# Optimization experiments

Hardware: AMD Instinct MI355X
Metric: run time of the kernel (lower is better)

## Reference

```python
import jax, jax.numpy as jnp
import numpy as np

ALPHA = 0.2  # LeakyReLU negative slope
NEG = -9e15


def _gat_heads(x, adj_mask, W, a):
    # x: (B,N,F); W: (H,F,O); a: (H,2O); adj_mask: (B,N,N) bool
    O = W.shape[-1]
    Wh = jnp.einsum('bnf,hfo->bhno', x, W)            # (B,H,N,O)
    e1 = jnp.einsum('bhno,ho->bhn', Wh, a[:, :O])     # Wh @ a[:O]
    e2 = jnp.einsum('bhno,ho->bhn', Wh, a[:, O:])     # Wh @ a[O:]
    e = jax.nn.leaky_relu(e1[:, :, :, None] + e2[:, :, None, :], ALPHA)  # (B,H,N,N)
    e = jnp.where(adj_mask[:, None], e, NEG)
    attn = jax.nn.softmax(e, axis=-1)
    return jnp.einsum('bhnm,bhmo->bhno', attn, Wh)    # (B,H,N,O)


def _gat_block(x, adj_mask, non_pad_mask, W_heads, a_heads, W_out, a_out):
    # multi-head layer, concat=True -> elu per head, then concat on feature dim
    h = jax.nn.elu(_gat_heads(x, adj_mask, W_heads, a_heads))  # (B,H,N,O)
    B, H, N, O = h.shape
    h = jnp.transpose(h, (0, 2, 1, 3)).reshape(B, N, H * O)
    h = h * non_pad_mask
    # out layer: single head, concat=False (no inner elu)
    h = _gat_heads(h, adj_mask, W_out[None], a_out[None])[:, 0]  # (B,N,noutput)
    h = h * non_pad_mask
    return jax.nn.elu(h)


def setup_inputs() -> dict:
    key = jax.random.key(0)
    ks = jax.random.split(key, 8)
    B, N = 32, 256
    vocab, F, O, H, OUT = 200, 300, 256, 8, 512
    fea = jax.random.randint(ks[0], (B, N), 0, vocab, dtype=jnp.int32)
    adj = jax.random.randint(ks[1], (B, N, N), 0, 2, dtype=jnp.int32)
    non_pad_mask = jnp.ones((B, N, 1), dtype=jnp.float32)
    embed = jax.random.normal(ks[2], (vocab, F), dtype=jnp.float32)
    W_heads = jax.random.normal(ks[3], (H, F, O), dtype=jnp.float32) / np.sqrt(F)
    a_heads = jax.random.normal(ks[4], (H, 2 * O), dtype=jnp.float32) / np.sqrt(2 * O)
    W_out = jax.random.normal(ks[5], (H * O, OUT), dtype=jnp.float32) / np.sqrt(H * O)
    a_out = jax.random.normal(ks[6], (2 * OUT,), dtype=jnp.float32) / np.sqrt(2 * OUT)
    return {"fea": fea, "adj": adj, "non_pad_mask": non_pad_mask, "embed": embed,
            "W_heads": W_heads, "a_heads": a_heads, "W_out": W_out, "a_out": a_out}


def reference(fea, adj, non_pad_mask, embed, W_heads, a_heads, W_out, a_out):
    adj_mask = adj > 0
    x = embed[fea]  # (B,N,F)
    # GAT_num = 1; dropout is identity in eval mode
    x = _gat_block(x, adj_mask, non_pad_mask, W_heads, a_heads, W_out, a_out)
    return x  # (B, N, 512)
```

## Files before the change

### kernel.cpp

```cpp
#include <hip/hip_runtime.h>
#include <math.h>


typedef _Float16 f16;
typedef __attribute__((ext_vector_type(8))) _Float16 f16x8;
typedef __attribute__((ext_vector_type(4))) _Float16 f16x4;
typedef __attribute__((ext_vector_type(4))) float f32x4;
typedef unsigned long long u64;

__device__ __forceinline__ void async16(const void* g, void* lds) {
  __builtin_amdgcn_global_load_lds(
      (const __attribute__((address_space(1))) void*)g,
      (__attribute__((address_space(3))) void*)lds, 16, 0, 0);
}

__global__ __launch_bounds__(256) void k_prep(const int* __restrict__ fea,
                                              const float* __restrict__ embed,
                                              const float* __restrict__ Whd,
                                              const float* __restrict__ Wo,
                                              const int* __restrict__ adj,
                                              f16* __restrict__ x16,
                                              f16* __restrict__ WcT,
                                              f16* __restrict__ WoT,
                                              float* __restrict__ e_all,
                                              u64* __restrict__ adjG) {
  int bid = blockIdx.x, tid = threadIdx.x;
  if (bid < 1280) {
    int idx = bid * 256 + tid;
    int row = idx / 40, c = idx % 40;
    int tok = fea[row];
    const float* eb = embed + (size_t)tok * 300;
    f16x8 v;
    if (c < 37) {
      float4 f0 = *(const float4*)&eb[c * 8];
      float4 f1 = *(const float4*)&eb[c * 8 + 4];
      v[0] = (f16)f0.x; v[1] = (f16)f0.y; v[2] = (f16)f0.z; v[3] = (f16)f0.w;
      v[4] = (f16)f1.x; v[5] = (f16)f1.y; v[6] = (f16)f1.z; v[7] = (f16)f1.w;
    } else {
#pragma unroll
      for (int j = 0; j < 8; ++j) {
        int t = c * 8 + j;
        v[j] = (f16)((t < 300) ? eb[t] : 0.f);
      }
    }
    *(f16x8*)&x16[(size_t)row * 320 + c * 8] = v;
  } else if (bid < 1920) {
    int r = bid - 1280;
    int zi = r * 256 + tid;
    if (zi < 16384) e_all[zi] = 0.f;
    __shared__ float tile[32][33];
    int bx = r % 10, q0 = r / 10;
    int by = q0 % 8, h = q0 / 8;
    int c = tid & 31, q = tid >> 5;
#pragma unroll
    for (int i = 0; i < 4; ++i) {
      int tt = q + i * 8;
      int t = bx * 32 + tt;
      float v = (t < 300) ? Whd[((size_t)h * 300 + t) * 256 + by * 32 + c] : 0.f;
      tile[tt][c] = v;
    }
    __syncthreads();
#pragma unroll
    for (int i = 0; i < 4; ++i) {
      int oo = q + i * 8;
      int gc = h * 256 + by * 32 + oo;
      WcT[(size_t)gc * 320 + bx * 32 + c] = (f16)tile[c][oo];
    }
  } else if (bid < 2944) {
    int r = bid - 1920;
    __shared__ float tile[32][33];
    int bx = r % 64, by = r / 64;
    int c = tid & 31, q = tid >> 5;
#pragma unroll
    for (int i = 0; i < 4; ++i) {
      int kk = q + i * 8;
      tile[kk][c] = Wo[((size_t)bx * 32 + kk) * 512 + by * 32 + c];
    }
    __syncthreads();
#pragma unroll
    for (int i = 0; i < 4; ++i) {
      int oo = q + i * 8;
      WoT[((size_t)by * 32 + oo) * 2048 + bx * 32 + c] = (f16)tile[c][oo];
    }
  } else {
    int r = bid - 2944;
    int wv = tid >> 6, ln = tid & 63;
    int row = r * 64 + wv * 16;
    const int* ar = adj + (size_t)row * 256;
#pragma unroll 4
    for (int i = 0; i < 16; ++i, ar += 256) {
      u64 m0 = __ballot(ar[ln] != 0);
      u64 m1 = __ballot(ar[64 + ln] != 0);
      u64 m2 = __ballot(ar[128 + ln] != 0);
      u64 m3 = __ballot(ar[192 + ln] != 0);
      if (ln == 0) {
        u64* d = &adjG[(size_t)(row + i) * 4];
        d[0] = m0; d[1] = m1; d[2] = m2; d[3] = m3;
      }
    }
  }
}

__global__ __launch_bounds__(512, 1) void k_l1(
    const f16* __restrict__ x16, const f16* __restrict__ WcT,
    const float* __restrict__ ah, const u64* __restrict__ adjG,
    const float* __restrict__ npm, f16* __restrict__ h1) {
  extern __shared__ __align__(16) char smem[];
  f16* AsB[2] = {(f16*)smem, (f16*)(smem + 65536)};
  f16* BsB[2] = {(f16*)(smem + 32768), (f16*)(smem + 98304)};
  char* WhB = smem;
  u64* adjB = (u64*)(smem + 131072);
  float* e1f = (float*)(smem + 139264);
  float* e2f = (float*)(smem + 140288);

  const int bid = blockIdx.x;
  const int h = (bid >> 3) & 7;
  const int b = (bid & 7) * 4 + (bid >> 6);
  const int tid = threadIdx.x;
  const int wave = tid >> 6, lane = tid & 63;
  const int wm = wave >> 2, wn = wave & 3;
  const int lrow = lane & 15, quad = lane >> 4;
  const int srow = lane >> 3;
  const int scol = ((lane & 7) ^ (lane >> 3)) * 8;
  const int l7 = lrow & 7;

  if (tid < 256) e1f[tid] = 0.f;
  else e2f[tid - 256] = 0.f;

  f32x4 acc[8][4] = {};
  const f16* Ag = x16 + (size_t)b * 256 * 320;
  const f16* Bg = WcT + (size_t)h * 256 * 320;

  async16((const char*)adjG + (size_t)b * 8192 + tid * 16, (char*)adjB + tid * 16);
#pragma unroll
  for (int j = 0; j < 4; ++j) {
    const int r0 = wave * 32 + j * 8;
    async16(Ag + (size_t)(r0 + srow) * 320 + scol, &AsB[0][r0 * 64]);
    async16(Bg + (size_t)(r0 + srow) * 320 + scol, &BsB[0][r0 * 64]);
  }
  __syncthreads();

#pragma unroll
  for (int t = 0; t < 5; ++t) {
    const f16* As = AsB[t & 1];
    const f16* Bs = BsB[t & 1];
    if (t < 4) {
      const int kn = (t + 1) * 64;
      f16* An = AsB[(t + 1) & 1];
      f16* Bn = BsB[(t + 1) & 1];
#pragma unroll
      for (int j = 0; j < 4; ++j) {
        const int r0 = wave * 32 + j * 8;
        async16(Ag + (size_t)(r0 + srow) * 320 + kn + scol, &An[r0 * 64]);
        async16(Bg + (size_t)(r0 + srow) * 320 + kn + scol, &Bn[r0 * 64]);
      }
    }
#pragma unroll
    for (int s = 0; s < 2; ++s) {
      const int sq = ((s * 4 + quad) ^ l7) * 8;
      f16x8 af[8], bf[4];
#pragma unroll
      for (int mt = 0; mt < 8; ++mt)
        af[mt] = *(const f16x8*)&As[(wm * 128 + mt * 16 + lrow) * 64 + sq];
#pragma unroll
      for (int nt = 0; nt < 4; ++nt)
        bf[nt] = *(const f16x8*)&Bs[(wn * 64 + nt * 16 + lrow) * 64 + sq];
#pragma unroll
      for (int mt = 0; mt < 8; ++mt)
#pragma unroll
        for (int nt = 0; nt < 4; ++nt)
          acc[mt][nt] = __builtin_amdgcn_mfma_f32_16x16x32_f16(af[mt], bf[nt], acc[mt][nt], 0, 0, 0);
    }
    __syncthreads();
  }

  float a1v[4], a2v[4];
#pragma unroll
  for (int nt = 0; nt < 4; ++nt) {
    const int o = wn * 64 + nt * 16 + lrow;
    a1v[nt] = ah[h * 512 + o];
    a2v[nt] = ah[h * 512 + 256 + o];
  }
#pragma unroll
  for (int mt = 0; mt < 8; ++mt) {
    const int n0 = wm * 128 + mt * 16 + quad * 4;
    const int q16 = n0 >> 3;
    const int hoff = (n0 & 4) ? 8 : 0;
    float s1[4] = {0.f, 0.f, 0.f, 0.f}, s2[4] = {0.f, 0.f, 0.f, 0.f};
#pragma unroll
    for (int nt = 0; nt < 4; ++nt) {
      const int o = wn * 64 + nt * 16 + lrow;
      f16x4 v;
#pragma unroll
      for (int r = 0; r < 4; ++r) {
        v[r] = (f16)acc[mt][nt][r];
        s1[r] += acc[mt][nt][r] * a1v[nt];
        s2[r] += acc[mt][nt][r] * a2v[nt];
      }
      *(f16x4*)(WhB + o * 512 + ((q16 ^ (o & 7)) * 16 + hoff)) = v;
    }
#pragma unroll
    for (int r = 0; r < 4; ++r)
#pragma unroll
      for (int m = 1; m < 16; m <<= 1) {
        s1[r] += __shfl_xor(s1[r], m);
        s2[r] += __shfl_xor(s2[r], m);
      }
    if (lrow == 0) {
#pragma unroll
      for (int r = 0; r < 4; ++r) {
        atomicAdd(&e1f[n0 + r], s1[r]);
        atomicAdd(&e2f[n0 + r], s2[r]);
      }
    }
  }
  __syncthreads();

  float4 e2q = *(const float4*)&e2f[lane * 4];
  float e2m = fmaxf(fmaxf(e2q.x, e2q.y), fmaxf(e2q.z, e2q.w));
#pragma unroll
  for (int m = 1; m < 64; m <<= 1) e2m = fmaxf(e2m, __shfl_xor(e2m, m));

  const int nb0 = wave * 32;
  const float er0 = e1f[nb0 + lrow];
  const float er1 = e1f[nb0 + 16 + lrow];
  float sh0 = er0 + e2m; sh0 = sh0 > 0.f ? sh0 : 0.2f * sh0;
  float sh1 = er1 + e2m; sh1 = sh1 > 0.f ? sh1 : 0.2f * sh1;
  u64 aw0[4], aw1[4];
#pragma unroll
  for (int q = 0; q < 4; ++q) {
    aw0[q] = adjB[(nb0 + lrow) * 4 + q];
    aw1[q] = adjB[(nb0 + 16 + lrow) * 4 + q];
  }

  f16x8 p0[8], p1[8];
  float ss0 = 0.f, ss1 = 0.f;
#pragma unroll
  for (int k0 = 0; k0 < 8; ++k0) {
    const float* e2p = &e2f[k0 * 32 + quad * 8];
    float4 ea = *(const float4*)e2p;
    float4 eb = *(const float4*)(e2p + 4);
    unsigned int b0 = (unsigned int)(aw0[k0 >> 1] >> ((k0 & 1) * 32 + quad * 8)) & 0xFFu;
    unsigned int b1 = (unsigned int)(aw1[k0 >> 1] >> ((k0 & 1) * 32 + quad * 8)) & 0xFFu;
    float e2arr[8] = {ea.x, ea.y, ea.z, ea.w, eb.x, eb.y, eb.z, eb.w};
    f16x8 q0, q1;
#pragma unroll
    for (int j = 0; j < 8; ++j) {
      float v = er0 + e2arr[j]; v = v > 0.f ? v : 0.2f * v;
      float p = (b0 >> j) & 1 ? __expf(v - sh0) : 0.f;
      ss0 += p; q0[j] = (f16)p;
      v = er1 + e2arr[j]; v = v > 0.f ? v : 0.2f * v;
      p = (b1 >> j) & 1 ? __expf(v - sh1) : 0.f;
      ss1 += p; q1[j] = (f16)p;
    }
    p0[k0] = q0; p1[k0] = q1;
  }
  ss0 += __shfl_xor(ss0, 16); ss0 += __shfl_xor(ss0, 32);
  ss1 += __shfl_xor(ss1, 16); ss1 += __shfl_xor(ss1, 32);
  const float rs0 = 1.f / ss0, rs1 = 1.f / ss1;
  const float pm0 = npm[b * 256 + nb0 + lrow];
  const float pm1 = npm[b * 256 + nb0 + 16 + lrow];
  f16* h1b0 = &h1[(size_t)(b * 256 + nb0 + lrow) * 2048 + h * 256];
  f16* h1b1 = &h1[(size_t)(b * 256 + nb0 + 16 + lrow) * 2048 + h * 256];
  const char* wp = WhB + (size_t)lrow * 512;

#pragma unroll 4
  for (int of = 0; of < 16; ++of) {
    f32x4 c0 = {}, c1 = {};
    const char* wo = wp + of * 8192;
#pragma unroll
    for (int k0 = 0; k0 < 8; ++k0) {
      f16x8 af = *(const f16x8*)(wo + (((k0 * 4 + quad) ^ l7) * 16));
      c0 = __builtin_amdgcn_mfma_f32_16x16x32_f16(af, p0[k0], c0, 0, 0, 0);
      c1 = __builtin_amdgcn_mfma_f32_16x16x32_f16(af, p1[k0], c1, 0, 0, 0);
    }
    const int o0 = of * 16 + quad * 4;
    f16x4 s0, s1;
#pragma unroll
    for (int r = 0; r < 4; ++r) {
      float v = c0[r] * rs0;
      v = v > 0.f ? v : (__expf(v) - 1.f);
      s0[r] = (f16)(v * pm0);
      v = c1[r] * rs1;
      v = v > 0.f ? v : (__expf(v) - 1.f);
      s1[r] = (f16)(v * pm1);
    }
    *(f16x4*)(h1b0 + o0) = s0;
    *(f16x4*)(h1b1 + o0) = s1;
  }
}

__global__ __launch_bounds__(256, 4) void k_gemm_sk(const f16* __restrict__ A,
                                                    const f16* __restrict__ BT,
                                                    f16* __restrict__ outSK,
                                                    const float* __restrict__ ao,
                                                    float* __restrict__ e12,
                                                    float* __restrict__ e22) {
  __shared__ f16 As[128 * 64];
  __shared__ f16 Bs[64 * 64];
  const int bid = blockIdx.x;
  const int xcd = bid & 7, j5 = bid >> 3;
  const int bx = j5 & 7;
  const int kz = (j5 >> 6) & 1;
  const int by = xcd * 8 + ((j5 >> 3) & 7);
  const int tid = threadIdx.x;
  const int wave = tid >> 6, lane = tid & 63;
  const int wm = wave >> 1, wn = wave & 1;
  const int lrow = lane & 15, quad = lane >> 4;
  const int srow = lane >> 3;
  const int scol = ((lane & 7) ^ (lane >> 3)) * 8;
  const int l7 = lrow & 7;

  f32x4 acc[4][2] = {};
  const f16* Ag = A + (size_t)by * 128 * 2048;
  const f16* Bg = BT + (size_t)bx * 64 * 2048;
  const int kbeg = kz * 1024;

  for (int k0 = kbeg; k0 < kbeg + 1024; k0 += 64) {
    __syncthreads();
#pragma unroll
    for (int j = 0; j < 4; ++j) {
      const int r0 = wave * 32 + j * 8;
      async16(Ag + (size_t)(r0 + srow) * 2048 + k0 + scol, &As[r0 * 64]);
    }
#pragma unroll
    for (int j = 0; j < 2; ++j) {
      const int r0 = wave * 16 + j * 8;
      async16(Bg + (size_t)(r0 + srow) * 2048 + k0 + scol, &Bs[r0 * 64]);
    }
    __syncthreads();
#pragma unroll
    for (int s = 0; s < 2; ++s) {
      const int sq = ((s * 4 + quad) ^ l7) * 8;
      f16x8 af[4], bf[2];
#pragma unroll
      for (int t = 0; t < 4; ++t)
        af[t] = *(const f16x8*)&As[(wm * 64 + t * 16 + lrow) * 64 + sq];
#pragma unroll
      for (int t = 0; t < 2; ++t)
        bf[t] = *(const f16x8*)&Bs[(wn * 32 + t * 16 + lrow) * 64 + sq];
#pragma unroll
      for (int mt = 0; mt < 4; ++mt)
#pragma unroll
        for (int nt = 0; nt < 2; ++nt)
          acc[mt][nt] = __builtin_amdgcn_mfma_f32_16x16x32_f16(af[mt], bf[nt], acc[mt][nt], 0, 0, 0);
    }
  }

  const int b = (by * 128) >> 8;
  const int nbase0 = (by * 128) & 255;
  f16* dst = outSK + (size_t)kz * 32 * 512 * 256;
#pragma unroll
  for (int mt = 0; mt < 4; ++mt) {
    const int nb = nbase0 + wm * 64 + mt * 16 + quad * 4;
#pragma unroll
    for (int nt = 0; nt < 2; ++nt) {
      const int gc = bx * 64 + wn * 32 + nt * 16 + lrow;
      f16x4 v;
#pragma unroll
      for (int r = 0; r < 4; ++r) v[r] = (f16)acc[mt][nt][r];
      *(f16x4*)&dst[((size_t)b * 512 + gc) * 256 + nb] = v;
    }
  }

  float a1v[2], a2v[2];
#pragma unroll
  for (int nt = 0; nt < 2; ++nt) {
    const int gc = bx * 64 + wn * 32 + nt * 16 + lrow;
    a1v[nt] = ao[gc];
    a2v[nt] = ao[512 + gc];
  }
#pragma unroll
  for (int mt = 0; mt < 4; ++mt) {
    float s1[4] = {0.f, 0.f, 0.f, 0.f}, s2[4] = {0.f, 0.f, 0.f, 0.f};
#pragma unroll
    for (int nt = 0; nt < 2; ++nt)
#pragma unroll
      for (int r = 0; r < 4; ++r) {
        s1[r] += acc[mt][nt][r] * a1v[nt];
        s2[r] += acc[mt][nt][r] * a2v[nt];
      }
#pragma unroll
    for (int r = 0; r < 4; ++r)
#pragma unroll
      for (int m = 1; m < 16; m <<= 1) {
        s1[r] += __shfl_xor(s1[r], m);
        s2[r] += __shfl_xor(s2[r], m);
      }
    if (lrow == 0) {
      const int nb = nbase0 + wm * 64 + mt * 16 + quad * 4;
#pragma unroll
      for (int r = 0; r < 4; ++r) {
        atomicAdd(&e12[b * 256 + nb + r], s1[r]);
        atomicAdd(&e22[b * 256 + nb + r], s2[r]);
      }
    }
  }
}

#define PSTRIDE 264

__global__ __launch_bounds__(256, 4) void k_attn2(
    const f16* __restrict__ sk, const float* __restrict__ e1g, const float* __restrict__ e2g,
    const u64* __restrict__ adjG, const float* __restrict__ npm, float* __restrict__ out) {
  int bid = blockIdx.x;
  int nt0 = (bid >> 3) & 3;
  int pair = (bid >> 5) * 8 + (bid & 7);
  int oh = pair >> 5, b = pair & 31;
  int n0 = nt0 * 64;
  __shared__ f16 P[64 * PSTRIDE];
  int tid = threadIdx.x;
  int wave = tid >> 6, lane = tid & 63;
  int lrow = lane & 15, quad = lane >> 4;

  const f16* Ag0 = sk + ((size_t)b * 512 + oh * 128) * 256;
  const f16* Ag1 = Ag0 + (size_t)32 * 512 * 256;
  f16x8 afp0[2], afp1[2];
#pragma unroll
  for (int mt = 0; mt < 2; ++mt) {
    size_t off = (size_t)(wave * 32 + mt * 16 + lrow) * 256 + quad * 8;
    afp0[mt] = *(const f16x8*)&Ag0[off];
    afp1[mt] = *(const f16x8*)&Ag1[off];
  }

  float4 e2v = *(const float4*)&e2g[b * 256 + lane * 4];
  float e2m = fmaxf(fmaxf(e2v.x, e2v.y), fmaxf(e2v.z, e2v.w));
#pragma unroll
  for (int m = 1; m < 64; m <<= 1) e2m = fmaxf(e2m, __shfl_xor(e2m, m));
#pragma unroll 4
  for (int i = 0; i < 16; ++i) {
    int row = i * 4 + wave;
    int gn = b * 256 + n0 + row;
    float er = e1g[b * 256 + n0 + row];
    float sh = er + e2m;
    sh = sh > 0.f ? sh : 0.2f * sh;
    u64 word = adjG[(size_t)gn * 4 + (lane >> 4)];
    unsigned int bits = (unsigned int)(word >> ((lane & 15) * 4)) & 0xFu;
    float p0, p1, p2, p3;
    {
      float v = er + e2v.x; v = v > 0.f ? v : 0.2f * v;
      p0 = bits & 1 ? __expf(v - sh) : 0.f;
      v = er + e2v.y; v = v > 0.f ? v : 0.2f * v;
      p1 = bits & 2 ? __expf(v - sh) : 0.f;
      v = er + e2v.z; v = v > 0.f ? v : 0.2f * v;
      p2 = bits & 4 ? __expf(v - sh) : 0.f;
      v = er + e2v.w; v = v > 0.f ? v : 0.2f * v;
      p3 = bits & 8 ? __expf(v - sh) : 0.f;
    }
    float sm = p0 + p1 + p2 + p3;
#pragma unroll
    for (int m = 1; m < 64; m <<= 1) sm += __shfl_xor(sm, m);
    float rs = 1.f / sm;
    f16x4 pw;
    pw[0] = (f16)(p0 * rs); pw[1] = (f16)(p1 * rs);
    pw[2] = (f16)(p2 * rs); pw[3] = (f16)(p3 * rs);
    *(f16x4*)&P[row * PSTRIDE + lane * 4] = pw;
  }
  __syncthreads();

  f32x4 acc[2][4] = {};
#pragma unroll
  for (int kk = 0; kk < 8; ++kk) {
    const int k0 = kk * 32;
    f16x8 af[2], bf[4];
#pragma unroll
    for (int mt = 0; mt < 2; ++mt) {
      if (kk == 0) {
        af[mt] = afp0[mt] + afp1[mt];
      } else {
        size_t off = (size_t)(wave * 32 + mt * 16 + lrow) * 256 + k0 + quad * 8;
        af[mt] = *(const f16x8*)&Ag0[off] + *(const f16x8*)&Ag1[off];
      }
    }
#pragma unroll
    for (int nt = 0; nt < 4; ++nt)
      bf[nt] = *(const f16x8*)&P[(nt * 16 + lrow) * PSTRIDE + k0 + quad * 8];
#pragma unroll
    for (int mt = 0; mt < 2; ++mt)
#pragma unroll
      for (int nt = 0; nt < 4; ++nt)
        acc[mt][nt] = __builtin_amdgcn_mfma_f32_16x16x32_f16(af[mt], bf[nt], acc[mt][nt], 0, 0, 0);
  }
#pragma unroll
  for (int nt = 0; nt < 4; ++nt) {
    int nloc = nt * 16 + lrow;
    int gn = b * 256 + n0 + nloc;
    float pm = npm[gn];
#pragma unroll
    for (int mt = 0; mt < 2; ++mt) {
      int o0 = oh * 128 + wave * 32 + mt * 16 + quad * 4;
      float4 st;
      float v0 = acc[mt][nt][0] * pm;
      float v1 = acc[mt][nt][1] * pm;
      float v2 = acc[mt][nt][2] * pm;
      float v3 = acc[mt][nt][3] * pm;
      st.x = v0 > 0.f ? v0 : (__expf(v0) - 1.f);
      st.y = v1 > 0.f ? v1 : (__expf(v1) - 1.f);
      st.z = v2 > 0.f ? v2 : (__expf(v2) - 1.f);
      st.w = v3 > 0.f ? v3 : (__expf(v3) - 1.f);
      *(float4*)&out[(size_t)gn * 512 + o0] = st;
    }
  }
}

extern "C" void kernel_launch(void* const* d_in, const int* in_sizes, int n_in,
                              void* d_out, int out_size, void* d_ws, size_t ws_size,
                              hipStream_t stream) {
  (void)in_sizes; (void)n_in; (void)out_size; (void)ws_size;
  const int*   fea   = (const int*)d_in[0];
  const int*   adj   = (const int*)d_in[1];
  const float* npm   = (const float*)d_in[2];
  const float* embed = (const float*)d_in[3];
  const float* Whd   = (const float*)d_in[4];
  const float* ah    = (const float*)d_in[5];
  const float* Wo    = (const float*)d_in[6];
  const float* ao    = (const float*)d_in[7];
  float* out = (float*)d_out;

  char* ws = (char*)d_ws;
  f16* x16  = (f16*)ws;  ws += (size_t)8192 * 320 * 2;
  f16* WcT  = (f16*)ws;  ws += (size_t)2048 * 320 * 2;
  f16* WoT  = (f16*)ws;  ws += (size_t)512 * 2048 * 2;
  f16* h1   = (f16*)ws;  ws += (size_t)8192 * 2048 * 2;
  f16* Wh2sk = (f16*)ws; ws += (size_t)2 * 32 * 512 * 256 * 2;
  float* e12 = (float*)ws; ws += (size_t)8192 * 4;
  float* e22 = (float*)ws; ws += (size_t)8192 * 4;
  u64* adjG = (u64*)ws;  ws += (size_t)8192 * 4 * 8;

  k_prep<<<3072, 256, 0, stream>>>(fea, embed, Whd, Wo, adj, x16, WcT, WoT, e12, adjG);

  k_l1<<<256, 512, 141312, stream>>>(x16, WcT, ah, adjG, npm, h1);

  k_gemm_sk<<<1024, 256, 0, stream>>>(h1, WoT, Wh2sk, ao, e12, e22);
  k_attn2<<<512, 256, 0, stream>>>(Wh2sk, e12, e22, adjG, npm, out);
}
```

Measured before the change: 179.1 us.

## Precompute W·a per head and split layer-1 blocks over output halves

Adds a prep stage that folds each head's attention vectors into the weights (W@a1, W@a2), so k_l1 gets e1/e2 as dot products of x with these vectors instead of reducing over the full Wh tile with shuffles and LDS atomics. k_l1 now splits each (batch, head) across two blocks, each covering half the output features, using 256 threads and about half the LDS, with two blocks per CU. The K-loop loses double buffering in exchange for higher occupancy. The attention softmax is recomputed in both halves and the e-values come from the fp16 x rather than the fp16-rounded Wh, which changes numerics slightly.

New measurement: 199.1 us. 11.2% more time.

```diff
diff --git a/kernel.cpp b/kernel.cpp
--- a/kernel.cpp
+++ b/kernel.cpp
@@ -19,11 +19,13 @@
                                               const float* __restrict__ Whd,
                                               const float* __restrict__ Wo,
                                               const int* __restrict__ adj,
+                                              const float* __restrict__ ah,
                                               f16* __restrict__ x16,
                                               f16* __restrict__ WcT,
                                               f16* __restrict__ WoT,
                                               float* __restrict__ e_all,
-                                              u64* __restrict__ adjG) {
+                                              u64* __restrict__ adjG,
+                                              float* __restrict__ w12G) {
   int bid = blockIdx.x, tid = threadIdx.x;
   if (bid < 1280) {
     int idx = bid * 256 + tid;
@@ -82,7 +84,7 @@
       int oo = q + i * 8;
       WoT[((size_t)by * 32 + oo) * 2048 + bx * 32 + c] = (f16)tile[c][oo];
     }
-  } else {
+  } else if (bid < 3072) {
     int r = bid - 2944;
     int wv = tid >> 6, ln = tid & 63;
     int row = r * 64 + wv * 16;
@@ -98,120 +100,126 @@
         d[0] = m0; d[1] = m1; d[2] = m2; d[3] = m3;
       }
     }
+  } else {
+    int hh = bid - 3072;
+    __shared__ float a1s[256], a2s[256];
+    a1s[tid] = ah[hh * 512 + tid];
+    a2s[tid] = ah[hh * 512 + 256 + tid];
+    __syncthreads();
+    for (int t = tid; t < 320; t += 256) {
+      float s1 = 0.f, s2 = 0.f;
+      if (t < 300) {
+        const float* wr = Whd + ((size_t)hh * 300 + t) * 256;
+#pragma unroll 4
+        for (int o = 0; o < 256; o += 4) {
+          float4 w4 = *(const float4*)&wr[o];
+          s1 += w4.x * a1s[o] + w4.y * a1s[o + 1] + w4.z * a1s[o + 2] + w4.w * a1s[o + 3];
+          s2 += w4.x * a2s[o] + w4.y * a2s[o + 1] + w4.z * a2s[o + 2] + w4.w * a2s[o + 3];
+        }
+      }
+      w12G[hh * 640 + t] = s1;
+      w12G[hh * 640 + 320 + t] = s2;
+    }
   }
 }
 
-__global__ __launch_bounds__(512, 1) void k_l1(
+__global__ __launch_bounds__(256, 2) void k_l1(
     const f16* __restrict__ x16, const f16* __restrict__ WcT,
-    const float* __restrict__ ah, const u64* __restrict__ adjG,
+    const float* __restrict__ w12G, const u64* __restrict__ adjG,
     const float* __restrict__ npm, f16* __restrict__ h1) {
   extern __shared__ __align__(16) char smem[];
-  f16* AsB[2] = {(f16*)smem, (f16*)(smem + 65536)};
-  f16* BsB[2] = {(f16*)(smem + 32768), (f16*)(smem + 98304)};
+  f16* As = (f16*)smem;
+  f16* Bs = (f16*)(smem + 32768);
   char* WhB = smem;
-  u64* adjB = (u64*)(smem + 131072);
-  float* e1f = (float*)(smem + 139264);
-  float* e2f = (float*)(smem + 140288);
+  u64* adjB = (u64*)(smem + 65536);
+  float* e2f = (float*)(smem + 73728);
+  float* e1f = (float*)(smem + 74752);
+  float* wl  = (float*)(smem + 75776);
 
   const int bid = blockIdx.x;
-  const int h = (bid >> 3) & 7;
-  const int b = (bid & 7) * 4 + (bid >> 6);
+  const int xcd = bid & 7, inner = bid >> 3;
+  const int oh = inner & 1;
+  const int h = (inner >> 1) & 7;
+  const int b = (inner >> 4) * 8 + xcd;
   const int tid = threadIdx.x;
   const int wave = tid >> 6, lane = tid & 63;
-  const int wm = wave >> 2, wn = wave & 3;
   const int lrow = lane & 15, quad = lane >> 4;
   const int srow = lane >> 3;
   const int scol = ((lane & 7) ^ (lane >> 3)) * 8;
   const int l7 = lrow & 7;
 
-  if (tid < 256) e1f[tid] = 0.f;
-  else e2f[tid - 256] = 0.f;
-
-  f32x4 acc[8][4] = {};
+  async16((const char*)adjG + (size_t)b * 8192 + tid * 16, (char*)adjB + tid * 16);
+  async16((const char*)adjG + (size_t)b * 8192 + 4096 + tid * 16,
+          (char*)adjB + 4096 + tid * 16);
+  if (tid < 160) async16((const char*)w12G + h * 2560 + tid * 16, (char*)wl + tid * 16);
+  __syncthreads();
+
+  {
+    const f16* xrow = x16 + ((size_t)b * 256 + tid) * 320;
+    float e1 = 0.f, e2 = 0.f;
+#pragma unroll 8
+    for (int c = 0; c < 40; ++c) {
+      f16x8 xv = *(const f16x8*)&xrow[c * 8];
+#pragma unroll
+      for (int j = 0; j < 8; ++j) {
+        float xf = (float)xv[j];
+        e1 += xf * wl[c * 8 + j];
+        e2 += xf * wl[320 + c * 8 + j];
+      }
+    }
+    e1f[tid] = e1;
+    e2f[tid] = e2;
+  }
+
+  f32x4 acc[4][8] = {};
   const f16* Ag = x16 + (size_t)b * 256 * 320;
-  const f16* Bg = WcT + (size_t)h * 256 * 320;
-
-  async16((const char*)adjG + (size_t)b * 8192 + tid * 16, (char*)adjB + tid * 16);
-#pragma unroll
-  for (int j = 0; j < 4; ++j) {
-    const int r0 = wave * 32 + j * 8;
-    async16(Ag + (size_t)(r0 + srow) * 320 + scol, &AsB[0][r0 * 64]);
-    async16(Bg + (size_t)(r0 + srow) * 320 + scol, &BsB[0][r0 * 64]);
-  }
-  __syncthreads();
-
-#pragma unroll
+  const f16* Bg = WcT + ((size_t)(h * 256 + oh * 128)) * 320;
+
   for (int t = 0; t < 5; ++t) {
-    const f16* As = AsB[t & 1];
-    const f16* Bs = BsB[t & 1];
-    if (t < 4) {
-      const int kn = (t + 1) * 64;
-      f16* An = AsB[(t + 1) & 1];
-      f16* Bn = BsB[(t + 1) & 1];
-#pragma unroll
-      for (int j = 0; j < 4; ++j) {
-        const int r0 = wave * 32 + j * 8;
-        async16(Ag + (size_t)(r0 + srow) * 320 + kn + scol, &An[r0 * 64]);
-        async16(Bg + (size_t)(r0 + srow) * 320 + kn + scol, &Bn[r0 * 64]);
-      }
-    }
+    const int k0 = t * 64;
+    __syncthreads();
+#pragma unroll
+    for (int j = 0; j < 8; ++j) {
+      const int r0 = wave * 64 + j * 8;
+      async16(Ag + (size_t)(r0 + srow) * 320 + k0 + scol, &As[r0 * 64]);
+    }
+#pragma unroll
+    for (int j = 0; j < 4; ++j) {
+      const int r0 = wave * 32 + j * 8;
+      async16(Bg + (size_t)(r0 + srow) * 320 + k0 + scol, &Bs[r0 * 64]);
+    }
+    __syncthreads();
 #pragma unroll
     for (int s = 0; s < 2; ++s) {
       const int sq = ((s * 4 + quad) ^ l7) * 8;
-      f16x8 af[8], bf[4];
-#pragma unroll
-      for (int mt = 0; mt < 8; ++mt)
-        af[mt] = *(const f16x8*)&As[(wm * 128 + mt * 16 + lrow) * 64 + sq];
-#pragma unroll
-      for (int nt = 0; nt < 4; ++nt)
-        bf[nt] = *(const f16x8*)&Bs[(wn * 64 + nt * 16 + lrow) * 64 + sq];
-#pragma unroll
-      for (int mt = 0; mt < 8; ++mt)
-#pragma unroll
-        for (int nt = 0; nt < 4; ++nt)
+      f16x8 af[4], bf[8];
+#pragma unroll
+      for (int mt = 0; mt < 4; ++mt)
+        af[mt] = *(const f16x8*)&As[(wave * 64 + mt * 16 + lrow) * 64 + sq];
+#pragma unroll
+      for (int nt = 0; nt < 8; ++nt)
+        bf[nt] = *(const f16x8*)&Bs[(nt * 16 + lrow) * 64 + sq];
+#pragma unroll
+      for (int mt = 0; mt < 4; ++mt)
+#pragma unroll
+        for (int nt = 0; nt < 8; ++nt)
           acc[mt][nt] = __builtin_amdgcn_mfma_f32_16x16x32_f16(af[mt], bf[nt], acc[mt][nt], 0, 0, 0);
     }
-    __syncthreads();
-  }
-
-  float a1v[4], a2v[4];
-#pragma unroll
-  for (int nt = 0; nt < 4; ++nt) {
-    const int o = wn * 64 + nt * 16 + lrow;
-    a1v[nt] = ah[h * 512 + o];
-    a2v[nt] = ah[h * 512 + 256 + o];
-  }
-#pragma unroll
-  for (int mt = 0; mt < 8; ++mt) {
-    const int n0 = wm * 128 + mt * 16 + quad * 4;
+  }
+  __syncthreads();
+
+#pragma unroll
+  for (int mt = 0; mt < 4; ++mt) {
+    const int n0 = wave * 64 + mt * 16 + quad * 4;
     const int q16 = n0 >> 3;
     const int hoff = (n0 & 4) ? 8 : 0;
-    float s1[4] = {0.f, 0.f, 0.f, 0.f}, s2[4] = {0.f, 0.f, 0.f, 0.f};
-#pragma unroll
-    for (int nt = 0; nt < 4; ++nt) {
-      const int o = wn * 64 + nt * 16 + lrow;
+#pragma unroll
+    for (int nt = 0; nt < 8; ++nt) {
+      const int o = nt * 16 + lrow;
       f16x4 v;
 #pragma unroll
-      for (int r = 0; r < 4; ++r) {
-        v[r] = (f16)acc[mt][nt][r];
-        s1[r] += acc[mt][nt][r] * a1v[nt];
-        s2[r] += acc[mt][nt][r] * a2v[nt];
-      }
+      for (int r = 0; r < 4; ++r) v[r] = (f16)acc[mt][nt][r];
       *(f16x4*)(WhB + o * 512 + ((q16 ^ (o & 7)) * 16 + hoff)) = v;
-    }
-#pragma unroll
-    for (int r = 0; r < 4; ++r)
-#pragma unroll
-      for (int m = 1; m < 16; m <<= 1) {
-        s1[r] += __shfl_xor(s1[r], m);
-        s2[r] += __shfl_xor(s2[r], m);
-      }
-    if (lrow == 0) {
-#pragma unroll
-      for (int r = 0; r < 4; ++r) {
-        atomicAdd(&e1f[n0 + r], s1[r]);
-        atomicAdd(&e2f[n0 + r], s2[r]);
-      }
     }
   }
   __syncthreads();
@@ -221,72 +229,77 @@
 #pragma unroll
   for (int m = 1; m < 64; m <<= 1) e2m = fmaxf(e2m, __shfl_xor(e2m, m));
 
-  const int nb0 = wave * 32;
-  const float er0 = e1f[nb0 + lrow];
-  const float er1 = e1f[nb0 + 16 + lrow];
-  float sh0 = er0 + e2m; sh0 = sh0 > 0.f ? sh0 : 0.2f * sh0;
-  float sh1 = er1 + e2m; sh1 = sh1 > 0.f ? sh1 : 0.2f * sh1;
-  u64 aw0[4], aw1[4];
-#pragma unroll
-  for (int q = 0; q < 4; ++q) {
-    aw0[q] = adjB[(nb0 + lrow) * 4 + q];
-    aw1[q] = adjB[(nb0 + 16 + lrow) * 4 + q];
-  }
-
-  f16x8 p0[8], p1[8];
-  float ss0 = 0.f, ss1 = 0.f;
+  float er[4], sh[4];
+  u64 aw[4][4];
+#pragma unroll
+  for (int g = 0; g < 4; ++g) {
+    int n = wave * 64 + g * 16 + lrow;
+    er[g] = e1f[n];
+    float s = er[g] + e2m;
+    sh[g] = s > 0.f ? s : 0.2f * s;
+#pragma unroll
+    for (int q = 0; q < 4; ++q) aw[g][q] = adjB[n * 4 + q];
+  }
+
+  f16x8 P[4][8];
+  float ss[4] = {0.f, 0.f, 0.f, 0.f};
 #pragma unroll
   for (int k0 = 0; k0 < 8; ++k0) {
     const float* e2p = &e2f[k0 * 32 + quad * 8];
     float4 ea = *(const float4*)e2p;
     float4 eb = *(const float4*)(e2p + 4);
-    unsigned int b0 = (unsigned int)(aw0[k0 >> 1] >> ((k0 & 1) * 32 + quad * 8)) & 0xFFu;
-    unsigned int b1 = (unsigned int)(aw1[k0 >> 1] >> ((k0 & 1) * 32 + quad * 8)) & 0xFFu;
     float e2arr[8] = {ea.x, ea.y, ea.z, ea.w, eb.x, eb.y, eb.z, eb.w};
-    f16x8 q0, q1;
-#pragma unroll
-    for (int j = 0; j < 8; ++j) {
-      float v = er0 + e2arr[j]; v = v > 0.f ? v : 0.2f * v;
-      float p = (b0 >> j) & 1 ? __expf(v - sh0) : 0.f;
-      ss0 += p; q0[j] = (f16)p;
-      v = er1 + e2arr[j]; v = v > 0.f ? v : 0.2f * v;
-      p = (b1 >> j) & 1 ? __expf(v - sh1) : 0.f;
-      ss1 += p; q1[j] = (f16)p;
-    }
-    p0[k0] = q0; p1[k0] = q1;
-  }
-  ss0 += __shfl_xor(ss0, 16); ss0 += __shfl_xor(ss0, 32);
-  ss1 += __shfl_xor(ss1, 16); ss1 += __shfl_xor(ss1, 32);
-  const float rs0 = 1.f / ss0, rs1 = 1.f / ss1;
-  const float pm0 = npm[b * 256 + nb0 + lrow];
-  const float pm1 = npm[b * 256 + nb0 + 16 + lrow];
-  f16* h1b0 = &h1[(size_t)(b * 256 + nb0 + lrow) * 2048 + h * 256];
-  f16* h1b1 = &h1[(size_t)(b * 256 + nb0 + 16 + lrow) * 2048 + h * 256];
-  const char* wp = WhB + (size_t)lrow * 512;
-
-#pragma unroll 4
-  for (int of = 0; of < 16; ++of) {
-    f32x4 c0 = {}, c1 = {};
-    const char* wo = wp + of * 8192;
+#pragma unroll
+    for (int g = 0; g < 4; ++g) {
+      unsigned int bits = (unsigned int)(aw[g][k0 >> 1] >> ((k0 & 1) * 32 + quad * 8)) & 0xFFu;
+      f16x8 q;
+#pragma unroll
+      for (int j = 0; j < 8; ++j) {
+        float v = er[g] + e2arr[j];
+        v = v > 0.f ? v : 0.2f * v;
+        float p = (bits >> j) & 1 ? __expf(v - sh[g]) : 0.f;
+        ss[g] += p;
+        q[j] = (f16)p;
+      }
+      P[g][k0] = q;
+    }
+  }
+  float rs[4], pm[4];
+  f16* hb[4];
+#pragma unroll
+  for (int g = 0; g < 4; ++g) {
+    ss[g] += __shfl_xor(ss[g], 16);
+    ss[g] += __shfl_xor(ss[g], 32);
+    rs[g] = 1.f / ss[g];
+    int n = wave * 64 + g * 16 + lrow;
+    pm[g] = npm[b * 256 + n];
+    hb[g] = &h1[((size_t)(b * 256 + n)) * 2048 + h * 256 + oh * 128];
+  }
+
+#pragma unroll 2
+  for (int of = 0; of < 8; ++of) {
+    const int ol = of * 16 + lrow;
+    const char* wo = WhB + ol * 512;
+    f32x4 c[4] = {};
 #pragma unroll
     for (int k0 = 0; k0 < 8; ++k0) {
-      f16x8 af = *(const f16x8*)(wo + (((k0 * 4 + quad) ^ l7) * 16));
-      c0 = __builtin_amdgcn_mfma_f32_16x16x32_f16(af, p0[k0], c0, 0, 0, 0);
-      c1 = __builtin_amdgcn_mfma_f32_16x16x32_f16(af, p1[k0], c1, 0, 0, 0);
+      f16x8 af = *(const f16x8*)(wo + (((k0 * 4 + quad) ^ (ol & 7)) * 16));
+#pragma unroll
+      for (int g = 0; g < 4; ++g)
+        c[g] = __builtin_amdgcn_mfma_f32_16x16x32_f16(af, P[g][k0], c[g], 0, 0, 0);
     }
     const int o0 = of * 16 + quad * 4;
-    f16x4 s0, s1;
-#pragma unroll
-    for (int r = 0; r < 4; ++r) {
-      float v = c0[r] * rs0;
-      v = v > 0.f ? v : (__expf(v) - 1.f);
-      s0[r] = (f16)(v * pm0);
-      v = c1[r] * rs1;
-      v = v > 0.f ? v : (__expf(v) - 1.f);
-      s1[r] = (f16)(v * pm1);
-    }
-    *(f16x4*)(h1b0 + o0) = s0;
-    *(f16x4*)(h1b1 + o0) = s1;
+#pragma unroll
+    for (int g = 0; g < 4; ++g) {
+      f16x4 st;
+#pragma unroll
+      for (int r = 0; r < 4; ++r) {
+        float v = c[g][r] * rs[g];
+        v = v > 0.f ? v : (__expf(v) - 1.f);
+        st[r] = (f16)(v * pm[g]);
+      }
+      *(f16x4*)(hb[g] + o0) = st;
+    }
   }
 }
 
@@ -526,10 +539,11 @@
   float* e12 = (float*)ws; ws += (size_t)8192 * 4;
   float* e22 = (float*)ws; ws += (size_t)8192 * 4;
   u64* adjG = (u64*)ws;  ws += (size_t)8192 * 4 * 8;
-
-  k_prep<<<3072, 256, 0, stream>>>(fea, embed, Whd, Wo, adj, x16, WcT, WoT, e12, adjG);
-
-  k_l1<<<256, 512, 141312, stream>>>(x16, WcT, ah, adjG, npm, h1);
+  float* w12G = (float*)ws; ws += (size_t)8 * 640 * 4;
+
+  k_prep<<<3080, 256, 0, stream>>>(fea, embed, Whd, Wo, adj, ah, x16, WcT, WoT, e12, adjG, w12G);
+
+  k_l1<<<512, 256, 78336, stream>>>(x16, WcT, w12G, adjG, npm, h1);
 
   k_gemm_sk<<<1024, 256, 0, stream>>>(h1, WoT, Wh2sk, ao, e12, e22);
   k_attn2<<<512, 256, 0, stream>>>(Wh2sk, e12, e22, adjG, npm, out);
```
